# Performance work log

Hardware: AMD Instinct MI355X
Metric: run time of the kernel (lower is better)

## Reference

```python
import jax, jax.numpy as jnp
import numpy as np

N = 50000      # nodes
E = 800000     # directed edges
D = 128        # in_dim == vertex_embed_dim
L = 3          # num_layers
EPS = 1e-5     # BatchNorm eps


def setup_inputs() -> dict:
    key = jax.random.key(0)
    k0, k1, k2 = jax.random.split(key, 3)
    x = jax.random.normal(k0, (N, D), dtype=jnp.float32)
    edge_index = jax.random.randint(k1, (2, E), 0, N, dtype=jnp.int32)
    Ws = jax.random.normal(k2, (L, D, D), dtype=jnp.float32) * 0.05
    bs = jnp.zeros((L, D), dtype=jnp.float32)
    gammas = jnp.ones((L, D), dtype=jnp.float32)
    betas = jnp.zeros((L, D), dtype=jnp.float32)
    return {"x": x, "edge_index": edge_index, "Ws": Ws, "bs": bs,
            "gammas": gammas, "betas": betas}


def reference(x, edge_index, Ws, bs, gammas, betas):
    # --- GCN normalization with self-loops (computed once, shared by all layers) ---
    loop = jnp.arange(N, dtype=edge_index.dtype)
    src = jnp.concatenate([edge_index[0], loop])   # [E+N]
    dst = jnp.concatenate([edge_index[1], loop])   # [E+N]
    deg = jax.ops.segment_sum(jnp.ones_like(dst, dtype=x.dtype), dst,
                              num_segments=N)       # in-degree of A + I
    dinv = jnp.where(deg > 0, jax.lax.rsqrt(deg), 0.0)
    norm = (dinv[src] * dinv[dst])[:, None]         # [E+N, 1]

    o = x
    h_v = [o]
    for i in range(L):
        h = o @ Ws[i]                                         # linear (no bias)
        msg = h[src] * norm                                   # gather + scale
        agg = jax.ops.segment_sum(msg, dst, num_segments=N)   # scatter-add
        agg = agg + bs[i]                                     # GCNConv bias
        # BatchNorm1d (training mode, biased batch stats)
        mu = jnp.mean(agg, axis=0)
        var = jnp.var(agg, axis=0)
        o = jax.nn.relu(gammas[i] * (agg - mu) * jax.lax.rsqrt(var + EPS)
                        + betas[i])
        h_v.append(o)
    return jnp.concatenate(h_v, axis=1)   # JK concat: [N, D*(L+1)]
```

## Files before the change

kernel.cpp:

```cpp
#include <hip/hip_runtime.h>


#define EPS_BN 1e-5f
#define NPW 2
#define REP 16

typedef short short8v __attribute__((ext_vector_type(8)));
typedef float float4v __attribute__((ext_vector_type(4)));

__device__ __forceinline__ unsigned bf16rne(float f){
  unsigned x = __float_as_uint(f);
  return (x + 0x7fffu + ((x >> 16) & 1u)) >> 16;
}
__device__ __forceinline__ float bflo(unsigned q){ return __uint_as_float(q << 16); }
__device__ __forceinline__ float bfhi(unsigned q){ return __uint_as_float(q & 0xffff0000u); }

__global__ void k_zero_i32(int* __restrict__ p, int n){
  int i = blockIdx.x*256 + threadIdx.x;
  if (i < n) p[i] = 0;
}

__global__ void k_scan1(const int* __restrict__ cnt, int* __restrict__ out,
                        int* __restrict__ blksum, float* __restrict__ dinv, int n){
  __shared__ int sh[256];
  int t = threadIdx.x;
  int base = blockIdx.x*1024 + t*4;
  int v[4];
  #pragma unroll
  for (int j=0;j<4;j++){
    int raw = (base+j < n) ? cnt[base+j] : 0;
    if (base+j < n) dinv[base+j] = rsqrtf((float)raw + 1.0f);
    v[j] = (base+j < n) ? ((raw + 7) & ~7) : 0;
  }
  int tsum = v[0]+v[1]+v[2]+v[3];
  sh[t] = tsum;
  __syncthreads();
  #pragma unroll
  for (int off=1; off<256; off<<=1){
    int x = (t>=off) ? sh[t-off] : 0;
    __syncthreads();
    sh[t] += x;
    __syncthreads();
  }
  if (t==255) blksum[blockIdx.x] = sh[255];
  int run = sh[t] - tsum;
  #pragma unroll
  for (int j=0;j<4;j++){ if (base+j < n) out[base+j] = run; run += v[j]; }
}

__global__ void k_scan3(int* __restrict__ out, int* __restrict__ rowcur,
                        const int* __restrict__ blksum, int nscan,
                        const int* __restrict__ cnt, int* __restrict__ colsrc, int n){
  __shared__ int lb[64];
  int t = threadIdx.x;
  if (t < nscan) lb[t] = blksum[t];
  __syncthreads();
  int i = blockIdx.x*256 + t;
  int myblk = i >> 10;
  int pre = 0, tot = 0;
  for (int k=0;k<nscan;k++){ int bv = lb[k]; tot += bv; if (k < myblk) pre += bv; }
  if (i < n){
    int r = out[i] + pre;
    out[i] = r;
    rowcur[i] = r;
    int c = cnt[i];
    int pc = (c + 7) & ~7;
    for (int p = r + c; p < r + pc; p++) colsrc[p] = 0;
  }
  if (i == 0) out[n] = tot;
}

__global__ void k_fill(const int* __restrict__ src, const int* __restrict__ dst,
                       const float* __restrict__ dinv,
                       int* __restrict__ rowcur, int* __restrict__ colsrc, int E){
  int e = blockIdx.x*256 + threadIdx.x;
  if (e < E){
    int d = dst[e];
    int pos = atomicAdd(&rowcur[d], 1);
    int s = src[e];
    colsrc[pos] = s | (int)(bf16rne(dinv[s]) << 16);
  }
}

template<int MODE>
__launch_bounds__(256)
__global__ void k_gemm(const void* __restrict__ Av, const float* __restrict__ W,
                       const float* __restrict__ statrep,
                       const float* __restrict__ gamma, const float* __restrict__ beta,
                       float* __restrict__ out, int colOff, unsigned* __restrict__ H2,
                       int n,
                       const int* __restrict__ dstE, int* __restrict__ cnt, int E,
                       int gemmGrid){
  const int t = threadIdx.x;
  if constexpr (MODE == 0){
    if ((int)blockIdx.x >= gemmGrid){
      int i = ((int)blockIdx.x - gemmGrid)*256 + t;
      if (i < E) atomicAdd(&cnt[dstE[i]], 1);
      return;
    }
  }
  __shared__ unsigned short Al[64*128];
  __shared__ unsigned short Wt[128*128];
  __shared__ float ssL[256];

  if constexpr (MODE == 1){
    if (t < 128){
      float s = 0.f, s2 = 0.f;
      #pragma unroll
      for (int r=0;r<REP;r++){
        s  += statrep[r*256 + t];
        s2 += statrep[r*256 + 128 + t];
      }
      float invn = 1.0f / (float)n;
      float mu  = s * invn;
      float var = s2 * invn - mu*mu;
      float rs  = rsqrtf(var + EPS_BN);
      float sc  = gamma[t] * rs;
      ssL[t]       = sc;
      ssL[128 + t] = beta[t] - mu * sc;
    }
    __syncthreads();
  }

  {
    int row = t >> 2;
    int q   = t & 3;
    int grow = blockIdx.x*64 + row;
    int gr  = grow > n-1 ? n-1 : grow;
    unsigned short* dstb = Al + row*128;
    int swz = (row & 7) << 3;
    if constexpr (MODE == 0){
      const float4* src = (const float4*)((const float*)Av + (size_t)gr*128 + q*32);
      #pragma unroll
      for (int c8=0; c8<4; c8++){
        float4 f0 = src[c8*2], f1 = src[c8*2+1];
        if (grow < n){
          float4* op = (float4*)(out + (size_t)grow*512 + q*32 + c8*8);
          op[0] = f0; op[1] = f1;
        }
        uint4 pk;
        pk.x = bf16rne(f0.x) | (bf16rne(f0.y)<<16);
        pk.y = bf16rne(f0.z) | (bf16rne(f0.w)<<16);
        pk.z = bf16rne(f1.x) | (bf16rne(f1.y)<<16);
        pk.w = bf16rne(f1.z) | (bf16rne(f1.w)<<16);
        int ke = q*32 + c8*8;
        *(uint4*)(dstb + (ke ^ swz)) = pk;
      }
    } else {
      const uint4* src = (const uint4*)((const unsigned*)Av + (size_t)gr*64 + q*16);
      #pragma unroll
      for (int c8=0; c8<4; c8++){
        uint4 ld = src[c8];
        int k0 = q*32 + c8*8;
        float4 o0, o1;
        o0.x = fmaxf(fmaf(bflo(ld.x), ssL[k0+0], ssL[128+k0+0]), 0.f);
        o0.y = fmaxf(fmaf(bfhi(ld.x), ssL[k0+1], ssL[128+k0+1]), 0.f);
        o0.z = fmaxf(fmaf(bflo(ld.y), ssL[k0+2], ssL[128+k0+2]), 0.f);
        o0.w = fmaxf(fmaf(bfhi(ld.y), ssL[k0+3], ssL[128+k0+3]), 0.f);
        o1.x = fmaxf(fmaf(bflo(ld.z), ssL[k0+4], ssL[128+k0+4]), 0.f);
        o1.y = fmaxf(fmaf(bfhi(ld.z), ssL[k0+5], ssL[128+k0+5]), 0.f);
        o1.z = fmaxf(fmaf(bflo(ld.w), ssL[k0+6], ssL[128+k0+6]), 0.f);
        o1.w = fmaxf(fmaf(bfhi(ld.w), ssL[k0+7], ssL[128+k0+7]), 0.f);
        if (grow < n){
          float4* op = (float4*)(out + (size_t)grow*512 + colOff + k0);
          op[0] = o0; op[1] = o1;
        }
        uint4 pk;
        pk.x = bf16rne(o0.x) | (bf16rne(o0.y)<<16);
        pk.y = bf16rne(o0.z) | (bf16rne(o0.w)<<16);
        pk.z = bf16rne(o1.x) | (bf16rne(o1.y)<<16);
        pk.w = bf16rne(o1.z) | (bf16rne(o1.w)<<16);
        *(uint4*)(dstb + (k0 ^ swz)) = pk;
      }
    }
  }
  {
    int nn = t & 127;
    int kh = t >> 7;
    int swz = (nn & 7) << 3;
    unsigned short* dstb = Wt + nn*128;
    #pragma unroll 4
    for (int i=0;i<32;i++){
      int k = (i*2 + kh)*2;
      float w0 = W[(size_t)k*128 + nn];
      float w1 = W[(size_t)(k+1)*128 + nn];
      *(unsigned*)(dstb + (k ^ swz)) = bf16rne(w0) | (bf16rne(w1)<<16);
    }
  }
  __syncthreads();

  const int w  = t >> 6;
  const int l  = t & 63;
  const int lo = l & 15, hi = l >> 4;

  const unsigned short* arow = Al + (w*16 + lo)*128;
  const int aswz = ((w*16 + lo) & 7) << 3;
  short8v a[4];
  #pragma unroll
  for (int kc=0;kc<4;kc++){
    int ke = kc*32 + hi*8;
    a[kc] = *(const short8v*)(arow + (ke ^ aswz));
  }

  float4v acc[8];
  #pragma unroll
  for (int ct=0;ct<8;ct++) acc[ct] = (float4v)(0.f);

  #pragma unroll
  for (int ct=0;ct<8;ct++){
    int col = ct*16 + lo;
    const unsigned short* brow = Wt + col*128;
    int bswz = (col & 7) << 3;
    #pragma unroll
    for (int kc=0;kc<4;kc++){
      int ke = kc*32 + hi*8;
      short8v b = *(const short8v*)(brow + (ke ^ bswz));
      acc[ct] = __builtin_amdgcn_mfma_f32_16x16x32_bf16(a[kc], b, acc[ct], 0, 0, 0);
    }
  }

  const int rbase = blockIdx.x*64 + w*16;
  #pragma unroll
  for (int ct=0;ct<8;ct++){
    int col = ct*16 + lo;
    #pragma unroll
    for (int r=0;r<4;r++){
      unsigned bits  = bf16rne(acc[ct][r]);
      unsigned other = (unsigned)__shfl_xor((int)bits, 1, 64);
      int grow = rbase + hi*4 + r;
      if (!(l & 1) && grow < n)
        H2[(size_t)grow*64 + (col>>1)] = bits | (other<<16);
    }
  }
}

#define GATH(d) (*(const unsigned*)(h2c + (size_t)(unsigned)(((d)&0xffff)<<8) + lane4))
#define FMA2(d,g) { float wv_=__uint_as_float((unsigned)(d)&0xffff0000u); \
                    a0=fmaf(wv_,bflo(g),a0); a1=fmaf(wv_,bfhi(g),a1); }
__launch_bounds__(256)
__global__ void k_agg(const unsigned* __restrict__ h2, const int* __restrict__ rowptr,
                      const int* __restrict__ colsrc, const float* __restrict__ dinv,
                      unsigned* __restrict__ aggsc,
                      float* __restrict__ statrep, int n){
  __shared__ float red[4*256];
  const char* h2c = (const char*)h2;
  const int lane  = threadIdx.x & 63;
  const unsigned lane4 = lane*4;
  const int wv   = __builtin_amdgcn_readfirstlane(threadIdx.x >> 6);
  const int v0   = (blockIdx.x*4 + wv) * NPW;
  const int4* c4 = (const int4*)colsrc;
  float s0=0.f, s1=0.f, q0s=0.f, q1s=0.f;
  #pragma unroll 1
  for (int vi=0; vi<NPW; vi++){
    int v = v0 + vi;
    if (v < n){
      int j   = __builtin_amdgcn_readfirstlane(rowptr[v]);
      int end = __builtin_amdgcn_readfirstlane(rowptr[v+1]);
      unsigned qs = *(const unsigned*)(h2c + (size_t)v*256 + lane4);
      float dv = dinv[v];
      float a0 = 0.f, a1 = 0.f;
      if (j < end){
        int4 A0 = c4[(j>>2)], A1 = c4[(j>>2)+1];
        unsigned g0=GATH(A0.x), g1=GATH(A0.y), g2=GATH(A0.z), g3=GATH(A0.w);
        unsigned g4=GATH(A1.x), g5=GATH(A1.y), g6=GATH(A1.z), g7=GATH(A1.w);
        #pragma unroll 1
        for (;;){
          int jn = j + 8;
          bool more = jn < end;
          int4 B0, B1;
          unsigned p0,p1,p2,p3,p4,p5,p6,p7;
          if (more){
            B0 = c4[(jn>>2)]; B1 = c4[(jn>>2)+1];
            p0=GATH(B0.x); p1=GATH(B0.y); p2=GATH(B0.z); p3=GATH(B0.w);
            p4=GATH(B1.x); p5=GATH(B1.y); p6=GATH(B1.z); p7=GATH(B1.w);
          }
          FMA2(A0.x,g0) FMA2(A0.y,g1) FMA2(A0.z,g2) FMA2(A0.w,g3)
          FMA2(A1.x,g4) FMA2(A1.y,g5) FMA2(A1.z,g6) FMA2(A1.w,g7)
          if (!more) break;
          A0=B0; A1=B1;
          g0=p0; g1=p1; g2=p2; g3=p3; g4=p4; g5=p5; g6=p6; g7=p7;
          j = jn;
        }
      }
      a0 = dv*(a0 + dv*bflo(qs));
      a1 = dv*(a1 + dv*bfhi(qs));
      aggsc[(size_t)v*64 + lane] = bf16rne(a0) | (bf16rne(a1) << 16);
      s0 += a0; q0s = fmaf(a0,a0,q0s);
      s1 += a1; q1s = fmaf(a1,a1,q1s);
    }
  }
  red[wv*256 + 2*lane]       = s0;
  red[wv*256 + 2*lane+1]     = s1;
  red[wv*256 + 128+2*lane]   = q0s;
  red[wv*256 + 128+2*lane+1] = q1s;
  __syncthreads();
  int t = threadIdx.x;
  float tot = red[t] + red[256+t] + red[512+t] + red[768+t];
  atomicAdd(&statrep[((blockIdx.x & (REP-1))<<8) + t], tot);
}

__launch_bounds__(256)
__global__ void k_bnfinal(const unsigned* __restrict__ aggsc,
                          const float* __restrict__ statrep,
                          const float* __restrict__ gamma, const float* __restrict__ beta,
                          float* __restrict__ out, int colOff, int n){
  __shared__ float ssL[256];
  int t = threadIdx.x;
  if (t < 128){
    float s = 0.f, s2 = 0.f;
    #pragma unroll
    for (int r=0;r<REP;r++){
      s  += statrep[r*256 + t];
      s2 += statrep[r*256 + 128 + t];
    }
    float invn = 1.0f / (float)n;
    float mu  = s * invn;
    float var = s2 * invn - mu*mu;
    float rs  = rsqrtf(var + EPS_BN);
    float sc  = gamma[t] * rs;
    ssL[t]       = sc;
    ssL[128 + t] = beta[t] - mu * sc;
  }
  __syncthreads();
  int i = blockIdx.x*256 + t;
  if (i >= n*16) return;
  int v = i >> 4, c = i & 15;
  uint4 ld = *(const uint4*)(aggsc + (size_t)v*64 + c*4);
  int k0 = c*8;
  float4 o0, o1;
  o0.x = fmaxf(fmaf(bflo(ld.x), ssL[k0+0], ssL[128+k0+0]), 0.f);
  o0.y = fmaxf(fmaf(bfhi(ld.x), ssL[k0+1], ssL[128+k0+1]), 0.f);
  o0.z = fmaxf(fmaf(bflo(ld.y), ssL[k0+2], ssL[128+k0+2]), 0.f);
  o0.w = fmaxf(fmaf(bfhi(ld.y), ssL[k0+3], ssL[128+k0+3]), 0.f);
  o1.x = fmaxf(fmaf(bflo(ld.z), ssL[k0+4], ssL[128+k0+4]), 0.f);
  o1.y = fmaxf(fmaf(bfhi(ld.z), ssL[k0+5], ssL[128+k0+5]), 0.f);
  o1.z = fmaxf(fmaf(bflo(ld.w), ssL[k0+6], ssL[128+k0+6]), 0.f);
  o1.w = fmaxf(fmaf(bfhi(ld.w), ssL[k0+7], ssL[128+k0+7]), 0.f);
  float4* op = (float4*)(out + (size_t)v*512 + colOff + k0);
  op[0] = o0; op[1] = o1;
}

extern "C" void kernel_launch(void* const* d_in, const int* in_sizes, int n_in,
                              void* d_out, int out_size, void* d_ws, size_t ws_size,
                              hipStream_t stream){
  const float* x      = (const float*)d_in[0];
  const int*   ei     = (const int*)d_in[1];
  const float* Ws     = (const float*)d_in[2];
  const float* gammas = (const float*)d_in[4];
  const float* betas  = (const float*)d_in[5];
  const int N = in_sizes[0] / 128;
  const int E = in_sizes[1] / 2;
  float* out = (float*)d_out;

  const int EPADCAP = E + 7*N + 8;

  char* w = (char*)d_ws;
  auto alloc = [&](size_t bytes)->char*{
    char* p = w; w += (bytes + 255) & ~(size_t)255; return p;
  };
  int*      cnt     = (int*)     alloc((size_t)N*4);
  float*    statrep = (float*)   alloc(3*REP*256*4);
  int*      rowptr  = (int*)     alloc((size_t)(N+1)*4);
  int*      rowcur  = (int*)     alloc((size_t)N*4);
  int*      blksum  = (int*)     alloc(64*4);
  int*      colsrc  = (int*)     alloc((size_t)EPADCAP*4);
  float*    dinv    = (float*)   alloc((size_t)N*4);
  unsigned* h2      = (unsigned*)alloc((size_t)N*64*4);
  unsigned* aggsc   = (unsigned*)alloc((size_t)N*64*4);

  const int* srcArr = ei;
  const int* dstArr = ei + E;

  const int nbN = (N + 255)/256;
  const int nbE = (E + 255)/256;
  const int nscan = (N + 1023)/1024;
  const int nz = (int)(((char*)statrep - (char*)cnt)/4) + 3*REP*256;

  const int gemmGrid = (N + 63)/64;
  const int aggGrid  = (N + 4*NPW-1)/(4*NPW);

  k_zero_i32<<<(nz + 255)/256,256,0,stream>>>(cnt, nz);
  k_gemm<0><<<gemmGrid + nbE,256,0,stream>>>(x, Ws, nullptr, nullptr, nullptr,
                                             out, 0, h2, N,
                                             dstArr, cnt, E, gemmGrid);
  k_scan1<<<nscan,256,0,stream>>>(cnt, rowptr, blksum, dinv, N);
  k_scan3<<<nbN,256,0,stream>>>(rowptr, rowcur, blksum, nscan, cnt, colsrc, N);
  k_fill<<<nbE,256,0,stream>>>(srcArr, dstArr, dinv, rowcur, colsrc, E);

  for (int l=0; l<3; l++){
    if (l > 0)
      k_gemm<1><<<gemmGrid,256,0,stream>>>(aggsc, Ws + (size_t)l*128*128,
                                           statrep + (l-1)*REP*256,
                                           gammas + (l-1)*128, betas + (l-1)*128,
                                           out, l*128, h2, N,
                                           nullptr, nullptr, 0, gemmGrid);
    k_agg<<<aggGrid,256,0,stream>>>(h2, rowptr, colsrc, dinv, aggsc,
                                    statrep + l*REP*256, N);
  }
  k_bnfinal<<<(N*16 + 255)/256,256,0,stream>>>(aggsc, statrep + 2*REP*256,
                                               gammas + 2*128, betas + 2*128,
                                               out, 3*128, N);
}
```

Measured before the change: 263.3 us.

## Pre-convert weights to bf16 once and load GEMM operands directly into registers

Adds a setup kernel, fused with the workspace zeroing, that converts all three weight matrices to bf16 in a transposed, MFMA-friendly layout once per call. The GEMM kernels then drop both LDS staging buffers and the block barrier. Each lane loads its A fragment straight from global memory into registers and reads B fragments from the pre-converted global weights, which are shared by all blocks and should stay in cache. This removes per-block fp32-to-bf16 conversion of W and the LDS traffic, at the cost of repeated, less coalesced global reads of W and A.

```diff
diff --git a/kernel.cpp b/kernel.cpp
--- a/kernel.cpp
+++ b/kernel.cpp
@@ -14,10 +14,27 @@
 }
 __device__ __forceinline__ float bflo(unsigned q){ return __uint_as_float(q << 16); }
 __device__ __forceinline__ float bfhi(unsigned q){ return __uint_as_float(q & 0xffff0000u); }
-
-__global__ void k_zero_i32(int* __restrict__ p, int n){
-  int i = blockIdx.x*256 + threadIdx.x;
-  if (i < n) p[i] = 0;
+__device__ __forceinline__ short8v as_s8(uint4 v){ return __builtin_bit_cast(short8v, v); }
+
+__global__ void k_setup(int* __restrict__ p, int nz, int nzb,
+                        const float* __restrict__ Ws, unsigned* __restrict__ Wbf){
+  int b = blockIdx.x;
+  if (b < nzb){
+    int i = b*256 + threadIdx.x;
+    if (i < nz) p[i] = 0;
+  } else {
+    int idx = (b - nzb)*256 + threadIdx.x;
+    if (idx < 3*128*64){
+      int l   = idx >> 13;
+      int r   = idx & 8191;
+      int col = r & 127;
+      int kp  = r >> 7;
+      const float* W = Ws + l*16384;
+      float w0 = W[(size_t)(2*kp)*128 + col];
+      float w1 = W[(size_t)(2*kp+1)*128 + col];
+      Wbf[l*8192 + col*64 + kp] = bf16rne(w0) | (bf16rne(w1) << 16);
+    }
+  }
 }
 
 __global__ void k_scan1(const int* __restrict__ cnt, int* __restrict__ out,
@@ -84,7 +101,7 @@
 
 template<int MODE>
 __launch_bounds__(256)
-__global__ void k_gemm(const void* __restrict__ Av, const float* __restrict__ W,
+__global__ void k_gemm(const void* __restrict__ Av, const unsigned* __restrict__ Wbf,
                        const float* __restrict__ statrep,
                        const float* __restrict__ gamma, const float* __restrict__ beta,
                        float* __restrict__ out, int colOff, unsigned* __restrict__ H2,
@@ -99,9 +116,7 @@
       return;
     }
   }
-  __shared__ unsigned short Al[64*128];
-  __shared__ unsigned short Wt[128*128];
-  __shared__ float ssL[256];
+  __shared__ __align__(16) float ssL[256];
 
   if constexpr (MODE == 1){
     if (t < 128){
@@ -122,99 +137,70 @@
     __syncthreads();
   }
 
-  {
-    int row = t >> 2;
-    int q   = t & 3;
-    int grow = blockIdx.x*64 + row;
-    int gr  = grow > n-1 ? n-1 : grow;
-    unsigned short* dstb = Al + row*128;
-    int swz = (row & 7) << 3;
-    if constexpr (MODE == 0){
-      const float4* src = (const float4*)((const float*)Av + (size_t)gr*128 + q*32);
-      #pragma unroll
-      for (int c8=0; c8<4; c8++){
-        float4 f0 = src[c8*2], f1 = src[c8*2+1];
-        if (grow < n){
-          float4* op = (float4*)(out + (size_t)grow*512 + q*32 + c8*8);
-          op[0] = f0; op[1] = f1;
-        }
-        uint4 pk;
-        pk.x = bf16rne(f0.x) | (bf16rne(f0.y)<<16);
-        pk.y = bf16rne(f0.z) | (bf16rne(f0.w)<<16);
-        pk.z = bf16rne(f1.x) | (bf16rne(f1.y)<<16);
-        pk.w = bf16rne(f1.z) | (bf16rne(f1.w)<<16);
-        int ke = q*32 + c8*8;
-        *(uint4*)(dstb + (ke ^ swz)) = pk;
-      }
-    } else {
-      const uint4* src = (const uint4*)((const unsigned*)Av + (size_t)gr*64 + q*16);
-      #pragma unroll
-      for (int c8=0; c8<4; c8++){
-        uint4 ld = src[c8];
-        int k0 = q*32 + c8*8;
-        float4 o0, o1;
-        o0.x = fmaxf(fmaf(bflo(ld.x), ssL[k0+0], ssL[128+k0+0]), 0.f);
-        o0.y = fmaxf(fmaf(bfhi(ld.x), ssL[k0+1], ssL[128+k0+1]), 0.f);
-        o0.z = fmaxf(fmaf(bflo(ld.y), ssL[k0+2], ssL[128+k0+2]), 0.f);
-        o0.w = fmaxf(fmaf(bfhi(ld.y), ssL[k0+3], ssL[128+k0+3]), 0.f);
-        o1.x = fmaxf(fmaf(bflo(ld.z), ssL[k0+4], ssL[128+k0+4]), 0.f);
-        o1.y = fmaxf(fmaf(bfhi(ld.z), ssL[k0+5], ssL[128+k0+5]), 0.f);
-        o1.z = fmaxf(fmaf(bflo(ld.w), ssL[k0+6], ssL[128+k0+6]), 0.f);
-        o1.w = fmaxf(fmaf(bfhi(ld.w), ssL[k0+7], ssL[128+k0+7]), 0.f);
-        if (grow < n){
-          float4* op = (float4*)(out + (size_t)grow*512 + colOff + k0);
-          op[0] = o0; op[1] = o1;
-        }
-        uint4 pk;
-        pk.x = bf16rne(o0.x) | (bf16rne(o0.y)<<16);
-        pk.y = bf16rne(o0.z) | (bf16rne(o0.w)<<16);
-        pk.z = bf16rne(o1.x) | (bf16rne(o1.y)<<16);
-        pk.w = bf16rne(o1.z) | (bf16rne(o1.w)<<16);
-        *(uint4*)(dstb + (k0 ^ swz)) = pk;
-      }
-    }
-  }
-  {
-    int nn = t & 127;
-    int kh = t >> 7;
-    int swz = (nn & 7) << 3;
-    unsigned short* dstb = Wt + nn*128;
-    #pragma unroll 4
-    for (int i=0;i<32;i++){
-      int k = (i*2 + kh)*2;
-      float w0 = W[(size_t)k*128 + nn];
-      float w1 = W[(size_t)(k+1)*128 + nn];
-      *(unsigned*)(dstb + (k ^ swz)) = bf16rne(w0) | (bf16rne(w1)<<16);
-    }
-  }
-  __syncthreads();
-
   const int w  = t >> 6;
   const int l  = t & 63;
   const int lo = l & 15, hi = l >> 4;
 
-  const unsigned short* arow = Al + (w*16 + lo)*128;
-  const int aswz = ((w*16 + lo) & 7) << 3;
+  const int grow = blockIdx.x*64 + w*16 + lo;
+  const int gr   = grow > n-1 ? n-1 : grow;
+  const bool valid = grow < n;
+
   short8v a[4];
   #pragma unroll
   for (int kc=0;kc<4;kc++){
-    int ke = kc*32 + hi*8;
-    a[kc] = *(const short8v*)(arow + (ke ^ aswz));
+    const int k0 = kc*32 + hi*8;
+    if constexpr (MODE == 0){
+      const float4* src = (const float4*)((const float*)Av + (size_t)gr*128 + k0);
+      float4 f0 = src[0], f1 = src[1];
+      if (valid){
+        float4* op = (float4*)(out + (size_t)grow*512 + k0);
+        op[0] = f0; op[1] = f1;
+      }
+      uint4 pk;
+      pk.x = bf16rne(f0.x) | (bf16rne(f0.y)<<16);
+      pk.y = bf16rne(f0.z) | (bf16rne(f0.w)<<16);
+      pk.z = bf16rne(f1.x) | (bf16rne(f1.y)<<16);
+      pk.w = bf16rne(f1.z) | (bf16rne(f1.w)<<16);
+      a[kc] = as_s8(pk);
+    } else {
+      uint4 ld = *(const uint4*)((const unsigned*)Av + (size_t)gr*64 + kc*16 + hi*4);
+      float4 sc0 = *(const float4*)(ssL + k0);
+      float4 sc1 = *(const float4*)(ssL + k0 + 4);
+      float4 sh0 = *(const float4*)(ssL + 128 + k0);
+      float4 sh1 = *(const float4*)(ssL + 128 + k0 + 4);
+      float4 o0, o1;
+      o0.x = fmaxf(fmaf(bflo(ld.x), sc0.x, sh0.x), 0.f);
+      o0.y = fmaxf(fmaf(bfhi(ld.x), sc0.y, sh0.y), 0.f);
+      o0.z = fmaxf(fmaf(bflo(ld.y), sc0.z, sh0.z), 0.f);
+      o0.w = fmaxf(fmaf(bfhi(ld.y), sc0.w, sh0.w), 0.f);
+      o1.x = fmaxf(fmaf(bflo(ld.z), sc1.x, sh1.x), 0.f);
+      o1.y = fmaxf(fmaf(bfhi(ld.z), sc1.y, sh1.y), 0.f);
+      o1.z = fmaxf(fmaf(bflo(ld.w), sc1.z, sh1.z), 0.f);
+      o1.w = fmaxf(fmaf(bfhi(ld.w), sc1.w, sh1.w), 0.f);
+      if (valid){
+        float4* op = (float4*)(out + (size_t)grow*512 + colOff + k0);
+        op[0] = o0; op[1] = o1;
+      }
+      uint4 pk;
+      pk.x = bf16rne(o0.x) | (bf16rne(o0.y)<<16);
+      pk.y = bf16rne(o0.z) | (bf16rne(o0.w)<<16);
+      pk.z = bf16rne(o1.x) | (bf16rne(o1.y)<<16);
+      pk.w = bf16rne(o1.z) | (bf16rne(o1.w)<<16);
+      a[kc] = as_s8(pk);
+    }
   }
 
   float4v acc[8];
   #pragma unroll
   for (int ct=0;ct<8;ct++) acc[ct] = (float4v)(0.f);
 
+  const unsigned short* Wb = (const unsigned short*)Wbf;
   #pragma unroll
   for (int ct=0;ct<8;ct++){
-    int col = ct*16 + lo;
-    const unsigned short* brow = Wt + col*128;
-    int bswz = (col & 7) << 3;
+    const unsigned short* brow = Wb + (ct*16 + lo)*128 + hi*8;
     #pragma unroll
     for (int kc=0;kc<4;kc++){
-      int ke = kc*32 + hi*8;
-      short8v b = *(const short8v*)(brow + (ke ^ bswz));
+      short8v b = *(const short8v*)(brow + kc*32);
       acc[ct] = __builtin_amdgcn_mfma_f32_16x16x32_bf16(a[kc], b, acc[ct], 0, 0, 0);
     }
   }
@@ -227,9 +213,9 @@
     for (int r=0;r<4;r++){
       unsigned bits  = bf16rne(acc[ct][r]);
       unsigned other = (unsigned)__shfl_xor((int)bits, 1, 64);
-      int grow = rbase + hi*4 + r;
-      if (!(l & 1) && grow < n)
-        H2[(size_t)grow*64 + (col>>1)] = bits | (other<<16);
+      int gr2 = rbase + hi*4 + r;
+      if (!(l & 1) && gr2 < n)
+        H2[(size_t)gr2*64 + (col>>1)] = bits | (other<<16);
     }
   }
 }
@@ -365,6 +351,7 @@
   int*      blksum  = (int*)     alloc(64*4);
   int*      colsrc  = (int*)     alloc((size_t)EPADCAP*4);
   float*    dinv    = (float*)   alloc((size_t)N*4);
+  unsigned* Wbf     = (unsigned*)alloc(3*128*64*4);
   unsigned* h2      = (unsigned*)alloc((size_t)N*64*4);
   unsigned* aggsc   = (unsigned*)alloc((size_t)N*64*4);
 
@@ -374,13 +361,15 @@
   const int nbN = (N + 255)/256;
   const int nbE = (E + 255)/256;
   const int nscan = (N + 1023)/1024;
-  const int nz = (int)(((char*)statrep - (char*)cnt)/4) + 3*REP*256;
+  const int nz  = (int)(((char*)statrep - (char*)cnt)/4) + 3*REP*256;
+  const int nzb = (nz + 255)/256;
+  const int nwp = (3*128*64 + 255)/256;
 
   const int gemmGrid = (N + 63)/64;
   const int aggGrid  = (N + 4*NPW-1)/(4*NPW);
 
-  k_zero_i32<<<(nz + 255)/256,256,0,stream>>>(cnt, nz);
-  k_gemm<0><<<gemmGrid + nbE,256,0,stream>>>(x, Ws, nullptr, nullptr, nullptr,
+  k_setup<<<nzb + nwp,256,0,stream>>>(cnt, nz, nzb, Ws, Wbf);
+  k_gemm<0><<<gemmGrid + nbE,256,0,stream>>>(x, Wbf, nullptr, nullptr, nullptr,
                                              out, 0, h2, N,
                                              dstArr, cnt, E, gemmGrid);
   k_scan1<<<nscan,256,0,stream>>>(cnt, rowptr, blksum, dinv, N);
@@ -389,7 +378,7 @@
 
   for (int l=0; l<3; l++){
     if (l > 0)
-      k_gemm<1><<<gemmGrid,256,0,stream>>>(aggsc, Ws + (size_t)l*128*128,
+      k_gemm<1><<<gemmGrid,256,0,stream>>>(aggsc, Wbf + l*8192,
                                            statrep + (l-1)*REP*256,
                                            gammas + (l-1)*128, betas + (l-1)*128,
                                            out, l*128, h2, N,
```

Result: no change. 260.0 us (-1.2%).
